# Optimization experiments

Hardware: AMD Instinct MI355X
Metric: run time of the kernel (lower is better)

Reference implementation:

```python
import jax, jax.numpy as jnp
import numpy as np

T = 36  # num_frames


def box_cxcywh_to_xyxy(b):
    cx, cy, w, h = jnp.split(b, 4, axis=-1)
    return jnp.concatenate([cx - 0.5 * w, cy - 0.5 * h, cx + 0.5 * w, cy + 0.5 * h], axis=-1)


def multi_iou(b1, b2):
    # b1: [Q,1,T,4], b2: [1,N,T,4], xyxy -> iou [Q,N,T]
    lt = jnp.maximum(b1[..., :2], b2[..., :2])
    rb = jnp.minimum(b1[..., 2:], b2[..., 2:])
    wh = jnp.clip(rb - lt, 0.0)
    inter = wh[..., 0] * wh[..., 1]
    a1 = (b1[..., 2] - b1[..., 0]) * (b1[..., 3] - b1[..., 1])
    a2 = (b2[..., 2] - b2[..., 0]) * (b2[..., 3] - b2[..., 1])
    union = a1 + a2 - inter
    return inter / union


def setup_inputs() -> dict:
    key = jax.random.key(0)
    k1, k2, k3, k4, k5, k6 = jax.random.split(key, 6)
    Q, N, C = 2048, 128, 42
    return {
        "pred_logits": jax.random.normal(k1, (T * Q, C), dtype=jnp.float32),
        "pred_boxes": jax.random.uniform(k2, (T * Q, 4), dtype=jnp.float32),
        "tgt_labels": jax.random.randint(k3, (N * T,), 0, C - 1),
        "tgt_boxes": jax.random.uniform(k4, (N * T, 4), dtype=jnp.float32),
        "tgt_valid": jax.random.randint(k5, (N * T,), 0, 2, dtype=jnp.int32),
        "tgt_original_valid": jax.random.randint(k6, (N * T,), 0, 2, dtype=jnp.int32),
    }


def reference(pred_logits, pred_boxes, tgt_labels, tgt_boxes, tgt_valid, tgt_original_valid):
    # Cost-matrix computation of SoftMaxHungarianMatcher (cost_class=cost_bbox=cost_giou=1,
    # use_giou=False, use_l1_distance_sum=False). The scipy linear_sum_assignment step is
    # CPU-serial / non-tensor and excluded; output is the [Q,N] cost fed to it.
    C = pred_logits.shape[-1]
    Q = pred_logits.shape[0] // T
    N = tgt_labels.shape[0] // T
    num_classes = C - 1  # background index

    probs = jax.nn.softmax(pred_logits, axis=-1).reshape(T, Q, C).transpose(1, 0, 2)  # [Q,T,C]
    boxes = pred_boxes.reshape(T, Q, 4).transpose(1, 0, 2)                            # [Q,T,4]
    tboxes = tgt_boxes.reshape(N, T, 4)
    valid = tgt_valid.reshape(N, T).astype(probs.dtype)                               # [N,T]
    ovalid = tgt_original_valid.reshape(N, T)
    ids = jnp.where(ovalid == 0, num_classes, tgt_labels.reshape(N, T))               # [N,T]

    denom = valid.sum(-1)  # [N] (per-instance count of valid frames)

    # class cost: -mean_t p(q, t, ids[n,t]) over valid frames
    gathered = probs[:, jnp.arange(T)[None, :], ids]                                  # [Q,N,T]
    class_cost = -(gathered * valid).sum(-1) / denom                                  # [Q,N]

    # bbox L1 cost: mean over (valid frames, 4 coords)
    l1 = jnp.abs(boxes[:, None] - tboxes[None]).mean(-1)                              # [Q,N,T]
    bbox_cost = (l1 * valid).sum(-1) / denom                                          # [Q,N]

    # IoU cost: -mean_t iou over valid frames
    iou = multi_iou(box_cxcywh_to_xyxy(boxes)[:, None], box_cxcywh_to_xyxy(tboxes)[None])
    iou_cost = -(iou * valid).sum(-1) / denom                                         # [Q,N]

    return class_cost + bbox_cost + iou_cost
```

## Files before the change

### kernel.cpp

```cpp
#include <hip/hip_runtime.h>
#include <hip/hip_bf16.h>


constexpr int T = 36;
constexpr int Q = 2048;
constexpr int C = 42;
constexpr int N = 128;

__global__ __launch_bounds__(256) void softmax_transpose_kernel(
    const float* __restrict__ logits, float* __restrict__ P2) {
  constexpr int QB = 64;
  constexpr int LS = C + 1;

  __shared__ float tile[QB * LS];
  __shared__ float s_max[4 * QB];
  __shared__ float s_sum[4 * QB];
  __shared__ float s_rinv[QB];

  const int t = blockIdx.y;
  const int q0 = blockIdx.x * QB;
  const int tid = threadIdx.x;

  const float* src = logits + ((size_t)t * Q + q0) * C;
  for (int i = tid; i < QB * C; i += 256) {
    int r = i / C, c = i % C;
    tile[r * LS + c] = src[i];
  }
  __syncthreads();

  const int part = tid >> 6;
  const int row = tid & 63;
  const int c0 = (part < 2) ? part * 11 : 22 + (part - 2) * 10;
  const int c1 = (part < 2) ? c0 + 11 : c0 + 10;

  float m = -1e30f;
  for (int c = c0; c < c1; ++c) m = fmaxf(m, tile[row * LS + c]);
  s_max[part * QB + row] = m;
  __syncthreads();

  m = fmaxf(fmaxf(s_max[row], s_max[QB + row]),
            fmaxf(s_max[2 * QB + row], s_max[3 * QB + row]));
  float s = 0.f;
  for (int c = c0; c < c1; ++c) {
    float e = __expf(tile[row * LS + c] - m);
    tile[row * LS + c] = e;
    s += e;
  }
  s_sum[part * QB + row] = s;
  __syncthreads();

  if (part == 0) {
    float stot = s_sum[row] + s_sum[QB + row] + s_sum[2 * QB + row] +
                 s_sum[3 * QB + row];
    s_rinv[row] = 1.f / stot;
  }
  __syncthreads();

  for (int i = tid; i < QB * C; i += 256) {
    int c = i >> 6;
    int r = i & 63;
    P2[(size_t)(t * C + c) * Q + q0 + r] = tile[r * LS + c] * s_rinv[r];
  }
}

__global__ __launch_bounds__(256, 4) void cost_kernel(
    const float* __restrict__ P2, const float* __restrict__ pred_boxes,
    const int* __restrict__ labels, const float* __restrict__ tboxes,
    const int* __restrict__ valid, const int* __restrict__ ovalid,
    float* __restrict__ out) {
  constexpr int NB = 4;
  constexpr int RES_STRIDE = NB + 1;

  const int q0 = blockIdx.x * 64;
  const int n0 = blockIdx.y * NB;
  const int tid = threadIdx.x;
  const int lane = tid & 63;
  const int sub = tid >> 6;
  const int q = q0 + lane;

  __shared__ float4 s_pb[T * 64];
  __shared__ float4 s_tb[NB * T];
  __shared__ int s_idv[NB * T];
  __shared__ float s_rden[NB];
  __shared__ float s_res[64 * RES_STRIDE];

  for (int i = tid; i < T * 64; i += 256) {
    int t = i >> 6, l = i & 63;
    s_pb[t * 64 + l] = ((const float4*)pred_boxes)[t * Q + q0 + l];
  }
  for (int i = tid; i < NB * T; i += 256) {
    int n = n0 + i / T;
    int t = i % T;
    int g = n * T + t;
    s_idv[i] = ((ovalid[g] == 0) ? (C - 1) : labels[g]) | (valid[g] << 8);
    s_tb[i] = ((const float4*)tboxes)[g];
  }
  if (tid < NB) {
    int n = n0 + tid;
    int s = 0;
    for (int t = 0; t < T; ++t) s += valid[n * T + t];
    s_rden[tid] = 1.f / (float)s;
  }
  __syncthreads();

  float acc = 0.f;
  const float* probs_base = P2 + q;

#pragma unroll
  for (int t = 0; t < T; ++t) {
    int pk = __builtin_amdgcn_readfirstlane(s_idv[sub * T + t]);
    int id = pk & 0xff;
    float v = (float)(pk >> 8);
    float p = probs_base[(size_t)(t * C + id) * Q];
    float4 pb = s_pb[t * 64 + lane];
    float4 tb = s_tb[sub * T + t];

    float l1 = 0.25f * (fabsf(pb.x - tb.x) + fabsf(pb.y - tb.y) +
                        fabsf(pb.z - tb.z) + fabsf(pb.w - tb.w));
    float px1 = pb.x - 0.5f * pb.z, py1 = pb.y - 0.5f * pb.w;
    float px2 = pb.x + 0.5f * pb.z, py2 = pb.y + 0.5f * pb.w;
    float tx1 = tb.x - 0.5f * tb.z, ty1 = tb.y - 0.5f * tb.w;
    float tx2 = tb.x + 0.5f * tb.z, ty2 = tb.y + 0.5f * tb.w;
    float iw = fmaxf(fminf(px2, tx2) - fmaxf(px1, tx1), 0.f);
    float ih = fmaxf(fminf(py2, ty2) - fmaxf(py1, ty1), 0.f);
    float inter = iw * ih;
    float uni = pb.z * pb.w + tb.z * tb.w - inter;
    acc += v * (l1 - p - inter / uni);
  }

  s_res[lane * RES_STRIDE + sub] = acc * s_rden[sub];
  __syncthreads();

  if (tid < 64) {
    float4 o;
    o.x = s_res[tid * RES_STRIDE + 0];
    o.y = s_res[tid * RES_STRIDE + 1];
    o.z = s_res[tid * RES_STRIDE + 2];
    o.w = s_res[tid * RES_STRIDE + 3];
    *(float4*)(out + (size_t)(q0 + tid) * N + n0) = o;
  }
}

extern "C" void kernel_launch(void* const* d_in, const int* in_sizes, int n_in,
                              void* d_out, int out_size, void* d_ws, size_t ws_size,
                              hipStream_t stream) {
  const float* logits = (const float*)d_in[0];
  const float* pboxes = (const float*)d_in[1];
  const int* labels = (const int*)d_in[2];
  const float* tboxes = (const float*)d_in[3];
  const int* valid = (const int*)d_in[4];
  const int* ovalid = (const int*)d_in[5];
  float* out = (float*)d_out;

  float* P2 = (float*)d_ws;

  dim3 g1(Q / 64, T);
  softmax_transpose_kernel<<<g1, 256, 0, stream>>>(logits, P2);

  dim3 g2(Q / 64, N / 4);
  cost_kernel<<<g2, 256, 0, stream>>>(P2, pboxes, labels, tboxes, valid, ovalid, out);
}
```

Before: 94.46 us.

## Split frame loop across two half-blocks and skip invalid frames in cost kernel

Doubles the cost kernel block to 512 threads and splits the 36 frames between two halves, reducing partial sums through shared memory. Frames whose valid flag is zero are now skipped by a wave-uniform branch, which avoids their probability gather and IoU arithmetic (about half the frames for random inputs). The shared-memory staging of predicted boxes is removed in favour of direct global loads. The trade-off is a loop that is no longer unrolled, an extra barrier and reduction step, and more global box traffic in place of LDS reuse.

Measured after the change: 87.90 us. 1.07x faster.

```diff
diff --git a/kernel.cpp b/kernel.cpp
--- a/kernel.cpp
+++ b/kernel.cpp
@@ -63,32 +63,28 @@
   }
 }
 
-__global__ __launch_bounds__(256, 4) void cost_kernel(
+__global__ __launch_bounds__(512) void cost_kernel(
     const float* __restrict__ P2, const float* __restrict__ pred_boxes,
     const int* __restrict__ labels, const float* __restrict__ tboxes,
     const int* __restrict__ valid, const int* __restrict__ ovalid,
     float* __restrict__ out) {
   constexpr int NB = 4;
-  constexpr int RES_STRIDE = NB + 1;
+  constexpr int RS = NB + 1;
 
   const int q0 = blockIdx.x * 64;
   const int n0 = blockIdx.y * NB;
   const int tid = threadIdx.x;
   const int lane = tid & 63;
-  const int sub = tid >> 6;
+  const int sub = (tid >> 6) & 3;
+  const int half = tid >> 8;
   const int q = q0 + lane;
 
-  __shared__ float4 s_pb[T * 64];
   __shared__ float4 s_tb[NB * T];
   __shared__ int s_idv[NB * T];
   __shared__ float s_rden[NB];
-  __shared__ float s_res[64 * RES_STRIDE];
+  __shared__ float s_res[2 * 64 * RS];
 
-  for (int i = tid; i < T * 64; i += 256) {
-    int t = i >> 6, l = i & 63;
-    s_pb[t * 64 + l] = ((const float4*)pred_boxes)[t * Q + q0 + l];
-  }
-  for (int i = tid; i < NB * T; i += 256) {
+  for (int i = tid; i < NB * T; i += 512) {
     int n = n0 + i / T;
     int t = i % T;
     int g = n * T + t;
@@ -105,38 +101,45 @@
 
   float acc = 0.f;
   const float* probs_base = P2 + q;
+  const int t_begin = half * (T / 2);
+  const int t_end = t_begin + (T / 2);
 
-#pragma unroll
-  for (int t = 0; t < T; ++t) {
-    int pk = __builtin_amdgcn_readfirstlane(s_idv[sub * T + t]);
-    int id = pk & 0xff;
-    float v = (float)(pk >> 8);
-    float p = probs_base[(size_t)(t * C + id) * Q];
-    float4 pb = s_pb[t * 64 + lane];
-    float4 tb = s_tb[sub * T + t];
+  for (int t = t_begin; t < t_end; ++t) {
+    int pk = s_idv[sub * T + t];
+    if (pk & 0x100) {
+      float4 pb = ((const float4*)pred_boxes)[t * Q + q];
+      float4 tb = s_tb[sub * T + t];
+      int id = pk & 0xff;
+      float p = probs_base[(size_t)(t * C + id) * Q];
 
-    float l1 = 0.25f * (fabsf(pb.x - tb.x) + fabsf(pb.y - tb.y) +
-                        fabsf(pb.z - tb.z) + fabsf(pb.w - tb.w));
-    float px1 = pb.x - 0.5f * pb.z, py1 = pb.y - 0.5f * pb.w;
-    float px2 = pb.x + 0.5f * pb.z, py2 = pb.y + 0.5f * pb.w;
-    float tx1 = tb.x - 0.5f * tb.z, ty1 = tb.y - 0.5f * tb.w;
-    float tx2 = tb.x + 0.5f * tb.z, ty2 = tb.y + 0.5f * tb.w;
-    float iw = fmaxf(fminf(px2, tx2) - fmaxf(px1, tx1), 0.f);
-    float ih = fmaxf(fminf(py2, ty2) - fmaxf(py1, ty1), 0.f);
-    float inter = iw * ih;
-    float uni = pb.z * pb.w + tb.z * tb.w - inter;
-    acc += v * (l1 - p - inter / uni);
+      float l1 = 0.25f * (fabsf(pb.x - tb.x) + fabsf(pb.y - tb.y) +
+                          fabsf(pb.z - tb.z) + fabsf(pb.w - tb.w));
+      float px1 = pb.x - 0.5f * pb.z, py1 = pb.y - 0.5f * pb.w;
+      float px2 = pb.x + 0.5f * pb.z, py2 = pb.y + 0.5f * pb.w;
+      float tx1 = tb.x - 0.5f * tb.z, ty1 = tb.y - 0.5f * tb.w;
+      float tx2 = tb.x + 0.5f * tb.z, ty2 = tb.y + 0.5f * tb.w;
+      float iw = fmaxf(fminf(px2, tx2) - fmaxf(px1, tx1), 0.f);
+      float ih = fmaxf(fminf(py2, ty2) - fmaxf(py1, ty1), 0.f);
+      float inter = iw * ih;
+      float uni = pb.z * pb.w + tb.z * tb.w - inter;
+      acc += l1 - p - inter / uni;
+    }
   }
 
-  s_res[lane * RES_STRIDE + sub] = acc * s_rden[sub];
+  s_res[half * (64 * RS) + lane * RS + sub] = acc;
+  __syncthreads();
+  if (half == 0) {
+    float tot = (acc + s_res[64 * RS + lane * RS + sub]) * s_rden[sub];
+    s_res[lane * RS + sub] = tot;
+  }
   __syncthreads();
 
   if (tid < 64) {
     float4 o;
-    o.x = s_res[tid * RES_STRIDE + 0];
-    o.y = s_res[tid * RES_STRIDE + 1];
-    o.z = s_res[tid * RES_STRIDE + 2];
-    o.w = s_res[tid * RES_STRIDE + 3];
+    o.x = s_res[tid * RS + 0];
+    o.y = s_res[tid * RS + 1];
+    o.z = s_res[tid * RS + 2];
+    o.w = s_res[tid * RS + 3];
     *(float4*)(out + (size_t)(q0 + tid) * N + n0) = o;
   }
 }
@@ -158,5 +161,5 @@
   softmax_transpose_kernel<<<g1, 256, 0, stream>>>(logits, P2);
 
   dim3 g2(Q / 64, N / 4);
-  cost_kernel<<<g2, 256, 0, stream>>>(P2, pboxes, labels, tboxes, valid, ovalid, out);
+  cost_kernel<<<g2, 512, 0, stream>>>(P2, pboxes, labels, tboxes, valid, ovalid, out);
 }
```
